# Kernel optimization log

Hardware: AMD Instinct MI355X
Metric: run time of the kernel (lower is better)

Reference implementation:

```python
import jax, jax.numpy as jnp
import numpy as np

N = 100000   # nodes
E = 400000   # edges (before self-loops)
G = 4000     # graphs in batch
F_IN = 32    # node_embedding
HID = 128    # hidden_channels
H = 3        # heads (hard-coded in module)
W3 = H * HID # 384, post-concat width
NC = 10      # num_classes
NL = 4       # num_layers
NEG_SLOPE = 0.2


def _lin(key, fan_in, fan_out):
    return jax.random.normal(key, (fan_in, fan_out), jnp.float32) * (1.0 / np.sqrt(fan_in))


def setup_inputs() -> dict:
    key = jax.random.key(0)
    ks = iter(jax.random.split(key, 40))
    x = jax.random.normal(next(ks), (N, F_IN), jnp.float32)
    edge_index = jax.random.randint(next(ks), (2, E), 0, N, dtype=jnp.int32)
    batch = jnp.sort(jax.random.randint(next(ks), (N,), 0, G, dtype=jnp.int32))
    inp = dict(x=x, edge_index=edge_index, batch=batch)
    # MLP stem
    inp['lin1_w'] = _lin(next(ks), F_IN, 2 * HID); inp['lin1_b'] = jnp.zeros((2 * HID,), jnp.float32)
    inp['lin2_w'] = _lin(next(ks), 2 * HID, HID);  inp['lin2_b'] = jnp.zeros((HID,), jnp.float32)
    # conv1: GATConv(HID -> HID, heads=3)
    inp['w0'] = _lin(next(ks), HID, W3)
    inp['as0'] = jax.random.normal(next(ks), (H, HID), jnp.float32) * 0.1
    inp['ad0'] = jax.random.normal(next(ks), (H, HID), jnp.float32) * 0.1
    inp['b0'] = jnp.zeros((W3,), jnp.float32)
    # remaining NL-1 convs: GATConv(W3 -> HID, heads=3), stacked
    inp['wl'] = jnp.stack([_lin(next(ks), W3, W3) for _ in range(NL - 1)])
    inp['asl'] = jax.random.normal(next(ks), (NL - 1, H, HID), jnp.float32) * 0.1
    inp['adl'] = jax.random.normal(next(ks), (NL - 1, H, HID), jnp.float32) * 0.1
    inp['bl'] = jnp.zeros((NL - 1, W3), jnp.float32)
    # batch norms (NL total, all width W3)
    inp['gamma'] = jnp.ones((NL, W3), jnp.float32)
    inp['beta'] = jnp.zeros((NL, W3), jnp.float32)
    # head
    inp['lin3_w'] = _lin(next(ks), W3, HID); inp['lin3_b'] = jnp.zeros((HID,), jnp.float32)
    inp['lin4_w'] = _lin(next(ks), HID, NC); inp['lin4_b'] = jnp.zeros((NC,), jnp.float32)
    return inp


def _gat(x, W, a_src, a_dst, bias, src, dst):
    # PyG GATConv, concat heads. x: [N, Fin]
    h = (x @ W).reshape(N, H, HID)                       # [N, H, C]
    es = jnp.einsum('nhc,hc->nh', h, a_src)              # [N, H]
    ed = jnp.einsum('nhc,hc->nh', h, a_dst)
    e = jax.nn.leaky_relu(es[src] + ed[dst], NEG_SLOPE)  # [Etot, H]
    m = jax.ops.segment_max(e, dst, num_segments=N)      # segment softmax over incoming edges
    p = jnp.exp(e - m[dst])
    s = jax.ops.segment_sum(p, dst, num_segments=N)
    alpha = p / s[dst]                                   # every node has a self-loop -> s>0
    out = jax.ops.segment_sum(alpha[:, :, None] * h[src], dst, num_segments=N)
    return out.reshape(N, W3) + bias


def _bn(x, g, b):
    mu = x.mean(0)
    var = x.var(0)
    return (x - mu) * jax.lax.rsqrt(var + 1e-5) * g + b


def reference(x, edge_index, batch, lin1_w, lin1_b, lin2_w, lin2_b,
              w0, as0, ad0, b0, wl, asl, adl, bl, gamma, beta,
              lin3_w, lin3_b, lin4_w, lin4_b):
    loop = jnp.arange(N, dtype=edge_index.dtype)
    src = jnp.concatenate([edge_index[0], loop])  # add_self_loops=True (PyG default)
    dst = jnp.concatenate([edge_index[1], loop])
    h = jax.nn.relu(x @ lin1_w + lin1_b)
    h = jax.nn.relu(h @ lin2_w + lin2_b)
    h = _gat(h, w0, as0, ad0, b0, src, dst)
    h = _bn(h, gamma[0], beta[0])
    for i in range(NL - 1):
        h = _gat(h, wl[i], asl[i], adl[i], bl[i], src, dst)
        h = _bn(h, gamma[i + 1], beta[i + 1])
    # global mean pool over graphs
    sums = jax.ops.segment_sum(h, batch, num_segments=G)
    cnt = jax.ops.segment_sum(jnp.ones((N,), h.dtype), batch, num_segments=G)
    g = sums / jnp.maximum(cnt, 1.0)[:, None]
    g = jax.nn.relu(g @ lin3_w + lin3_b)
    logits = g @ lin4_w + lin4_b
    return jax.nn.log_softmax(logits, axis=-1)
```

## Files before the change

kernel.cpp:

```cpp
#include <hip/hip_runtime.h>

#define NN      100000
#define NN2     100096
#define NE      400000
#define ETOT    500000
#define NG      4000
#define W3D     384
#define HIDD    128
#define NCLS    10
#define NSLICE  256

typedef unsigned short u16;
typedef unsigned int   u32;
typedef unsigned long long u64;
typedef __attribute__((ext_vector_type(8))) short short8;
typedef __attribute__((ext_vector_type(4))) float f32x4;

static __device__ __forceinline__ float bf2f(u16 u) {
  return __uint_as_float(((u32)u) << 16);
}
static __device__ __forceinline__ float bflo(u32 u) {
  return __uint_as_float(u << 16);
}
static __device__ __forceinline__ float bfhi(u32 u) {
  return __uint_as_float(u & 0xffff0000u);
}
static __device__ __forceinline__ u16 f2b(float f) {
  u32 u = __float_as_uint(f);
  u32 r = (u + 0x7fffu + ((u >> 16) & 1u)) >> 16;
  return (u16)r;
}

static __device__ __forceinline__ void llds16(const u16* g, u16* l) {
  __builtin_amdgcn_global_load_lds(
      (const __attribute__((address_space(1))) void*)(u64)(const void*)g,
      (__attribute__((address_space(3))) void*)(u64)(void*)l, 16, 0, 0);
}

__global__ void mg_zero_out(float* out, int n) {
  int i = blockIdx.x * 256 + threadIdx.x;
  if (i < n) out[i] = 0.f;
}

__global__ void mg_cvt_x(const float* __restrict__ x, u16* __restrict__ Xb) {
  int idx = blockIdx.x * 256 + threadIdx.x;
  if (idx >= NN2 * 64) return;
  int row = idx >> 6, col = idx & 63;
  Xb[idx] = (row < NN && col < 32) ? f2b(x[row * 32 + col]) : (u16)0;
}

__global__ void mg_transpose_pad(const float* __restrict__ in, u16* __restrict__ out,
                                 int K, int Nn, int Kpad) {
  int idx = blockIdx.x * 256 + threadIdx.x;
  if (idx >= Nn * Kpad) return;
  int n = idx / Kpad, k = idx - n * Kpad;
  out[idx] = (k < K) ? f2b(in[k * Nn + n]) : (u16)0;
}

__global__ void mg_fold_w(const u16* __restrict__ Wt, const float* __restrict__ scale,
                          const float* __restrict__ shift, u16* __restrict__ Wp,
                          float* __restrict__ bp) {
  __shared__ float red[128];
  int j = blockIdx.x, t = threadIdx.x;
  const u16* src = Wt + (size_t)j * W3D;
  u16* dst = Wp + (size_t)j * W3D;
  float acc = 0.f;
  for (int k = t; k < W3D; k += 128) {
    float w = bf2f(src[k]);
    dst[k] = f2b(w * scale[k]);
    acc += w * shift[k];
  }
  red[t] = acc; __syncthreads();
  for (int off = 64; off; off >>= 1) {
    if (t < off) red[t] += red[t + off];
    __syncthreads();
  }
  if (t == 0) bp[j] = red[0];
}

__global__ void mg_edge_histo(const int* __restrict__ ei, int* __restrict__ deg) {
  int e = blockIdx.x * 256 + threadIdx.x;
  if (e >= ETOT) return;
  int d = (e < NE) ? ei[NE + e] : (e - NE);
  atomicAdd(&deg[d], 1);
}

__global__ void mg_scan1(const int* __restrict__ in, int* __restrict__ bsum, int n) {
  __shared__ int sd[256];
  int tid = threadIdx.x;
  int base = blockIdx.x * 1024 + tid * 4;
  int s = 0;
#pragma unroll
  for (int j = 0; j < 4; ++j) { int i = base + j; if (i < n) s += in[i]; }
  sd[tid] = s; __syncthreads();
  for (int off = 128; off > 0; off >>= 1) {
    if (tid < off) sd[tid] += sd[tid + off];
    __syncthreads();
  }
  if (tid == 0) bsum[blockIdx.x] = sd[0];
}

__global__ void mg_scan2(int* __restrict__ bsum, int nb) {
  __shared__ int sd[256];
  int tid = threadIdx.x;
  int v = (tid < nb) ? bsum[tid] : 0;
  sd[tid] = v; __syncthreads();
  for (int off = 1; off < 256; off <<= 1) {
    int t = (tid >= off) ? sd[tid - off] : 0;
    __syncthreads();
    sd[tid] += t;
    __syncthreads();
  }
  if (tid < nb) bsum[tid] = sd[tid] - v;
}

__global__ void mg_scan3(const int* __restrict__ in, const int* __restrict__ bexcl,
                         int* __restrict__ out, int n) {
  __shared__ int sd[256];
  int tid = threadIdx.x;
  int base = blockIdx.x * 1024 + tid * 4;
  int loc[4]; int s = 0;
#pragma unroll
  for (int j = 0; j < 4; ++j) { int i = base + j; loc[j] = (i < n) ? in[i] : 0; s += loc[j]; }
  sd[tid] = s; __syncthreads();
  for (int off = 1; off < 256; off <<= 1) {
    int t = (tid >= off) ? sd[tid - off] : 0;
    __syncthreads();
    sd[tid] += t;
    __syncthreads();
  }
  int run = sd[tid] - s + bexcl[blockIdx.x];
#pragma unroll
  for (int j = 0; j < 4; ++j) {
    int i = base + j;
    if (i < n) { out[i] = run; run += loc[j]; if (i == n - 1) out[n] = run; }
  }
}

__global__ void mg_edge_scatter(const int* __restrict__ ei, int* __restrict__ fill,
                                int* __restrict__ colsrc) {
  int e = blockIdx.x * 256 + threadIdx.x;
  if (e >= ETOT) return;
  int s, d;
  if (e < NE) { s = ei[e]; d = ei[NE + e]; } else { s = e - NE; d = s; }
  int pos = atomicAdd(&fill[d], 1);
  colsrc[pos] = s;
}

__global__ void mg_graph_ptr(const int* __restrict__ batch, int* __restrict__ gptr) {
  int g = blockIdx.x * 256 + threadIdx.x;
  if (g > NG) return;
  if (g == NG) { gptr[NG] = NN; return; }
  int lo = 0, hi = NN;
  while (lo < hi) { int mid = (lo + hi) >> 1; if (batch[mid] < g) lo = mid + 1; else hi = mid; }
  gptr[g] = lo;
}

#define GBM 128
#define GBN 128
#define GBK 64
#define CP  136

__global__ __launch_bounds__(256) void mg_gemm(
    const u16* __restrict__ Ag, const u16* __restrict__ Bt,
    int Mstore, int Nn, int K,
    u16* __restrict__ Cb, const float* __restrict__ bias, int relu,
    const float* __restrict__ asrc, const float* __restrict__ adst,
    float* __restrict__ aes, float* __restrict__ aed) {
  __shared__ u16 lds[32768];
  int tid = threadIdx.x;
  int n0 = blockIdx.x * GBN, m0 = blockIdx.y * GBM;
  int lane = tid & 63, wv = tid >> 6;
  int mw = (wv & 1) * 64, nw = (wv >> 1) * 64;
  int lr = lane & 15, lq = lane >> 4;
  int sr = lane & 7, scl = lane >> 3;

  f32x4 acc[4][4];
#pragma unroll
  for (int mi = 0; mi < 4; ++mi)
#pragma unroll
    for (int ni = 0; ni < 4; ++ni) acc[mi][ni] = (f32x4){0.f, 0.f, 0.f, 0.f};

  const u16* aB = Ag + (size_t)m0 * K + scl * 8;
  const u16* bB = Bt + (size_t)n0 * K + scl * 8;
  int niter = K / GBK;

#pragma unroll
  for (int j = 0; j < 4; ++j) {
    int g = wv * 4 + j, grow = g * 8 + sr;
    llds16(aB + (size_t)grow * K, lds + g * 512);
    llds16(bB + (size_t)grow * K, lds + 16384 + g * 512);
  }

  for (int it = 0; it < niter; ++it) {
    __syncthreads();
    if (it + 1 < niter) {
      int k0 = (it + 1) * GBK, b = (it + 1) & 1;
#pragma unroll
      for (int j = 0; j < 4; ++j) {
        int g = wv * 4 + j, grow = g * 8 + sr;
        llds16(aB + (size_t)grow * K + k0, lds + b * 8192 + g * 512);
        llds16(bB + (size_t)grow * K + k0, lds + 16384 + b * 8192 + g * 512);
      }
    }
    const u16* Al = lds + (it & 1) * 8192;
    const u16* Bl = lds + 16384 + (it & 1) * 8192;
#pragma unroll
    for (int kk = 0; kk < GBK; kk += 32) {
      int ca = (kk >> 3) + lq;
      short8 af[4], bfr[4];
#pragma unroll
      for (int mi = 0; mi < 4; ++mi) {
        int r = mw + mi * 16 + lr;
        af[mi] = *(const short8*)(Al + (r >> 3) * 512 + ca * 64 + (r & 7) * 8);
      }
#pragma unroll
      for (int ni = 0; ni < 4; ++ni) {
        int r = nw + ni * 16 + lr;
        bfr[ni] = *(const short8*)(Bl + (r >> 3) * 512 + ca * 64 + (r & 7) * 8);
      }
#pragma unroll
      for (int mi = 0; mi < 4; ++mi)
#pragma unroll
        for (int ni = 0; ni < 4; ++ni)
          acc[mi][ni] = __builtin_amdgcn_mfma_f32_16x16x32_bf16(af[mi], bfr[ni], acc[mi][ni], 0, 0, 0);
    }
    __syncthreads();
  }

  float bvv[4];
#pragma unroll
  for (int ni = 0; ni < 4; ++ni)
    bvv[ni] = bias ? bias[n0 + nw + ni * 16 + lr] : 0.f;

#pragma unroll
  for (int mi = 0; mi < 4; ++mi)
#pragma unroll
    for (int ni = 0; ni < 4; ++ni) {
      int cl = nw + ni * 16 + lr;
      int rb = mw + mi * 16 + lq * 4;
#pragma unroll
      for (int r = 0; r < 4; ++r) {
        float v = acc[mi][ni][r] + bvv[ni];
        if (relu) v = fmaxf(v, 0.f);
        lds[(rb + r) * CP + cl] = f2b(v);
      }
    }
  __syncthreads();

  int rowl = tid >> 1, half = (tid & 1) * 64;
  const u16* src = lds + rowl * CP + half;
  uint4 creg[8];
#pragma unroll
  for (int j = 0; j < 8; ++j) creg[j] = *(const uint4*)(src + j * 8);
  u16* gout = Cb + (size_t)(m0 + rowl) * Nn + n0 + half;
#pragma unroll
  for (int j = 0; j < 8; ++j) *(uint4*)(gout + j * 8) = creg[j];

  if (aes) {
    const float* ap = asrc + n0 + half;
    const float* dp = adst + n0 + half;
    float se = 0.f, de = 0.f;
#pragma unroll
    for (int j = 0; j < 8; ++j) {
      float4 a0 = *(const float4*)(ap + j * 8);
      float4 a1 = *(const float4*)(ap + j * 8 + 4);
      float4 d0 = *(const float4*)(dp + j * 8);
      float4 d1 = *(const float4*)(dp + j * 8 + 4);
      uint4 rv = creg[j];
      float v0 = bflo(rv.x), v1 = bfhi(rv.x), v2 = bflo(rv.y), v3 = bfhi(rv.y);
      float v4 = bflo(rv.z), v5 = bfhi(rv.z), v6 = bflo(rv.w), v7 = bfhi(rv.w);
      se += v0 * a0.x + v1 * a0.y + v2 * a0.z + v3 * a0.w
          + v4 * a1.x + v5 * a1.y + v6 * a1.z + v7 * a1.w;
      de += v0 * d0.x + v1 * d0.y + v2 * d0.z + v3 * d0.w
          + v4 * d1.x + v5 * d1.y + v6 * d1.z + v7 * d1.w;
    }
    se += __shfl_xor(se, 1);
    de += __shfl_xor(de, 1);
    int row = m0 + rowl;
    if ((tid & 1) == 0 && row < Mstore) {
      aes[row * 4 + blockIdx.x] = se;
      aed[row * 4 + blockIdx.x] = de;
    }
  }
}

__global__ __launch_bounds__(256) void mg_aggregate(
    const u16* __restrict__ B, const float* __restrict__ es,
    const float* __restrict__ ed, const int* __restrict__ rowptr,
    const int* __restrict__ colsrc, const float* __restrict__ bias,
    u16* __restrict__ A, float* __restrict__ stats) {
  __shared__ float bS[4 * W3D];
  __shared__ float bQ[4 * W3D];
  int wv = threadIdx.x >> 6, lane = threadIdx.x & 63;
  if (lane < 48) {
    int h = lane >> 4;
    int cc = lane * 8;
    float4 bv0 = *(const float4*)(bias + cc);
    float4 bv1 = *(const float4*)(bias + cc + 4);
    float stS[8], stQ[8];
#pragma unroll
    for (int j = 0; j < 8; ++j) { stS[j] = 0.f; stQ[j] = 0.f; }
#pragma unroll
    for (int sub = 0; sub < 2; ++sub) {
      int n = blockIdx.x * 8 + wv * 2 + sub;
      int r0 = rowptr[n], r1 = rowptr[n + 1];
      float4 edv = *(const float4*)(ed + 4 * n);
      float4 esn = *(const float4*)(es + 4 * n);
      float s0 = esn.x + edv.x; s0 = (s0 > 0.f) ? s0 : 0.2f * s0;
      float s1 = esn.y + edv.y; s1 = (s1 > 0.f) ? s1 : 0.2f * s1;
      float s2 = esn.z + edv.z; s2 = (s2 > 0.f) ? s2 : 0.2f * s2;
      float mh  = (h == 0) ? s0 : ((h == 1) ? s1 : s2);
      float edh = (h == 0) ? edv.x : ((h == 1) ? edv.y : edv.z);
      float accv[8];
#pragma unroll
      for (int j = 0; j < 8; ++j) accv[j] = 0.f;
      float ssum = 0.f;
      int sA = __builtin_amdgcn_readfirstlane(colsrc[r0]);
      float4 evA = *(const float4*)(es + 4 * sA);
      uint4  rvA = *(const uint4*)(B + (size_t)sA * W3D + cc);
      float4 evB = evA; uint4 rvB = rvA;
      if (r0 + 1 < r1) {
        int sB = __builtin_amdgcn_readfirstlane(colsrc[r0 + 1]);
        evB = *(const float4*)(es + 4 * sB);
        rvB = *(const uint4*)(B + (size_t)sB * W3D + cc);
      }
      for (int r = r0; r < r1; ++r) {
        float4 ev = evA; uint4 rv = rvA;
        evA = evB; rvA = rvB;
        if (r + 2 < r1) {
          int sC = __builtin_amdgcn_readfirstlane(colsrc[r + 2]);
          evB = *(const float4*)(es + 4 * sC);
          rvB = *(const uint4*)(B + (size_t)sC * W3D + cc);
        }
        float e = ((h == 0) ? ev.x : ((h == 1) ? ev.y : ev.z)) + edh;
        e = (e > 0.f) ? e : 0.2f * e;
        float p = __expf(e - mh);
        ssum += p;
        accv[0] += p * bflo(rv.x); accv[1] += p * bfhi(rv.x);
        accv[2] += p * bflo(rv.y); accv[3] += p * bfhi(rv.y);
        accv[4] += p * bflo(rv.z); accv[5] += p * bfhi(rv.z);
        accv[6] += p * bflo(rv.w); accv[7] += p * bfhi(rv.w);
      }
      float inv = 1.0f / ssum;
      float v[8];
      v[0] = accv[0] * inv + bv0.x; v[1] = accv[1] * inv + bv0.y;
      v[2] = accv[2] * inv + bv0.z; v[3] = accv[3] * inv + bv0.w;
      v[4] = accv[4] * inv + bv1.x; v[5] = accv[5] * inv + bv1.y;
      v[6] = accv[6] * inv + bv1.z; v[7] = accv[7] * inv + bv1.w;
      uint4 st;
      st.x = (u32)f2b(v[0]) | ((u32)f2b(v[1]) << 16);
      st.y = (u32)f2b(v[2]) | ((u32)f2b(v[3]) << 16);
      st.z = (u32)f2b(v[4]) | ((u32)f2b(v[5]) << 16);
      st.w = (u32)f2b(v[6]) | ((u32)f2b(v[7]) << 16);
      *(uint4*)(A + (size_t)n * W3D + cc) = st;
#pragma unroll
      for (int j = 0; j < 8; ++j) { stS[j] += v[j]; stQ[j] += v[j] * v[j]; }
    }
    *(float4*)(bS + wv * W3D + cc)     = (float4){stS[0], stS[1], stS[2], stS[3]};
    *(float4*)(bS + wv * W3D + cc + 4) = (float4){stS[4], stS[5], stS[6], stS[7]};
    *(float4*)(bQ + wv * W3D + cc)     = (float4){stQ[0], stQ[1], stQ[2], stQ[3]};
    *(float4*)(bQ + wv * W3D + cc + 4) = (float4){stQ[4], stQ[5], stQ[6], stQ[7]};
  }
  __syncthreads();
  for (int t = threadIdx.x; t < W3D; t += 256) {
    float s = 0.f, q = 0.f;
#pragma unroll
    for (int w = 0; w < 4; ++w) { s += bS[w * W3D + t]; q += bQ[w * W3D + t]; }
    float* sl = stats + (size_t)(blockIdx.x & (NSLICE - 1)) * 768;
    atomicAdd(&sl[t], s);
    atomicAdd(&sl[W3D + t], q);
  }
}

__global__ void mg_bn_finalize(const float* __restrict__ stats, const float* __restrict__ gamma,
                               const float* __restrict__ beta, float* __restrict__ scale,
                               float* __restrict__ shift) {
  int c = threadIdx.x;
  float s = 0.f, q = 0.f;
  for (int b = 0; b < NSLICE; ++b) { s += stats[b * 768 + c]; q += stats[b * 768 + W3D + c]; }
  const float invN = 1.0f / (float)NN;
  float mu = s * invN;
  float var = fmaxf(q * invN - mu * mu, 0.f);
  float inv = rsqrtf(var + 1e-5f);
  float g = gamma[c], be = beta[c];
  scale[c] = g * inv;
  shift[c] = be - mu * g * inv;
}

__global__ void mg_pool(const u16* __restrict__ A, const float* __restrict__ scale,
                        const float* __restrict__ shift, const int* __restrict__ gptr,
                        float* __restrict__ pooled) {
  int g = blockIdx.x, c = threadIdx.x;
  int r0 = gptr[g], r1 = gptr[g + 1];
  float acc = 0.f;
  for (int n = r0; n < r1; ++n) acc += bf2f(A[(size_t)n * W3D + c]);
  int cnt = r1 - r0;
  float v = (cnt > 0) ? (acc / (float)cnt) * scale[c] + shift[c] : 0.f;
  pooled[g * W3D + c] = v;
}

__global__ void mg_head(const float* __restrict__ pooled, const float* __restrict__ w3,
                        const float* __restrict__ b3, const float* __restrict__ w4,
                        const float* __restrict__ b4, float* __restrict__ out) {
  __shared__ float p[W3D];
  __shared__ float g2[HIDD];
  __shared__ float lg[NCLS];
  int g = blockIdx.x, t = threadIdx.x;
  for (int i = t; i < W3D; i += 128) p[i] = pooled[g * W3D + i];
  __syncthreads();
  float acc = 0.f;
  for (int k = 0; k < W3D; ++k) acc += p[k] * w3[k * HIDD + t];
  g2[t] = fmaxf(acc + b3[t], 0.f);
  __syncthreads();
  if (t < NCLS) {
    float a = 0.f;
    for (int k = 0; k < HIDD; ++k) a += g2[k] * w4[k * NCLS + t];
    lg[t] = a + b4[t];
  }
  __syncthreads();
  if (t < NCLS) {
    float m = -1e30f;
#pragma unroll
    for (int j = 0; j < NCLS; ++j) m = fmaxf(m, lg[j]);
    float se = 0.f;
#pragma unroll
    for (int j = 0; j < NCLS; ++j) se += __expf(lg[j] - m);
    out[g * NCLS + t] = lg[t] - m - __logf(se);
  }
}

extern "C" void kernel_launch(void* const* d_in, const int* in_sizes, int n_in,
                              void* d_out, int out_size, void* d_ws, size_t ws_size,
                              hipStream_t stream) {
  const float* x     = (const float*)d_in[0];
  const int*   ei    = (const int*)d_in[1];
  const int*   batch = (const int*)d_in[2];
  const float* w1    = (const float*)d_in[3];
  const float* b1    = (const float*)d_in[4];
  const float* w2    = (const float*)d_in[5];
  const float* b2    = (const float*)d_in[6];
  const float* w0    = (const float*)d_in[7];
  const float* as0   = (const float*)d_in[8];
  const float* ad0   = (const float*)d_in[9];
  const float* b0    = (const float*)d_in[10];
  const float* wl    = (const float*)d_in[11];
  const float* asl   = (const float*)d_in[12];
  const float* adl   = (const float*)d_in[13];
  const float* bl    = (const float*)d_in[14];
  const float* gamma = (const float*)d_in[15];
  const float* beta  = (const float*)d_in[16];
  const float* w3    = (const float*)d_in[17];
  const float* b3    = (const float*)d_in[18];
  const float* w4    = (const float*)d_in[19];
  const float* b4    = (const float*)d_in[20];
  float* out = (float*)d_out;

  char* w = (char*)d_ws;
  auto alloc = [&](size_t bytes) -> void* {
    void* p = (void*)w;
    w += (bytes + 255) & ~(size_t)255;
    return p;
  };
  u16*   P      = (u16*)alloc((size_t)NN2 * W3D * 2);
  u16*   Q      = (u16*)alloc((size_t)NN2 * W3D * 2);
  float* es     = (float*)alloc((size_t)NN * 4 * 4);
  float* ed     = (float*)alloc((size_t)NN * 4 * 4);
  int*   deg    = (int*)alloc((size_t)NN * 4);
  int*   rowptr = (int*)alloc((size_t)(NN + 1) * 4);
  int*   fill   = (int*)alloc((size_t)NN * 4);
  int*   colsrc = (int*)alloc((size_t)ETOT * 4);
  int*   bsum   = (int*)alloc(256 * 4);
  float* stats  = (float*)alloc((size_t)NSLICE * 768 * 4);
  float* scale  = (float*)alloc(W3D * 4);
  float* shift  = (float*)alloc(W3D * 4);
  float* bprime = (float*)alloc(W3D * 4);
  int*   gptr   = (int*)alloc((size_t)(NG + 1) * 4);
  float* pooled = (float*)alloc((size_t)NG * W3D * 4);
  u16*   W1T    = (u16*)alloc(256 * 64 * 2);
  u16*   W2T    = (u16*)alloc(128 * 256 * 2);
  u16*   W0T    = (u16*)alloc(384 * 128 * 2);
  u16*   WlT    = (u16*)alloc((size_t)3 * 384 * 384 * 2);
  u16*   WpT    = (u16*)alloc((size_t)384 * 384 * 2);
  u16*   Xb     = Q;

  if ((size_t)(w - (char*)d_ws) > ws_size) {
    mg_zero_out<<<(out_size + 255) / 256, 256, 0, stream>>>(out, out_size);
    return;
  }

  mg_cvt_x<<<(NN2 * 64 + 255) / 256, 256, 0, stream>>>(x, Xb);
  mg_transpose_pad<<<(256 * 64 + 255) / 256, 256, 0, stream>>>(w1, W1T, 32, 256, 64);
  mg_transpose_pad<<<(128 * 256 + 255) / 256, 256, 0, stream>>>(w2, W2T, 256, 128, 256);
  mg_transpose_pad<<<(384 * 128 + 255) / 256, 256, 0, stream>>>(w0, W0T, 128, 384, 128);
  for (int i = 0; i < 3; ++i)
    mg_transpose_pad<<<(384 * 384 + 255) / 256, 256, 0, stream>>>(
        wl + (size_t)i * 384 * 384, WlT + (size_t)i * 384 * 384, 384, 384, 384);

  hipMemsetAsync(deg, 0, (size_t)NN * 4, stream);
  mg_edge_histo<<<(ETOT + 255) / 256, 256, 0, stream>>>(ei, deg);
  int nb = (NN + 1023) / 1024;
  mg_scan1<<<nb, 256, 0, stream>>>(deg, bsum, NN);
  mg_scan2<<<1, 256, 0, stream>>>(bsum, nb);
  mg_scan3<<<nb, 256, 0, stream>>>(deg, bsum, rowptr, NN);
  hipMemcpyAsync(fill, rowptr, (size_t)NN * 4, hipMemcpyDeviceToDevice, stream);
  mg_edge_scatter<<<(ETOT + 255) / 256, 256, 0, stream>>>(ei, fill, colsrc);
  mg_graph_ptr<<<(NG + 1 + 255) / 256, 256, 0, stream>>>(batch, gptr);

  dim3 blk(256);
  int mtiles = NN2 / GBM;

  mg_gemm<<<dim3(2, mtiles), blk, 0, stream>>>(Xb, W1T, NN, 256, 64,
                                               P, b1, 1,
                                               nullptr, nullptr, nullptr, nullptr);
  mg_gemm<<<dim3(1, mtiles), blk, 0, stream>>>(P, W2T, NN, 128, 256,
                                               Q, b2, 1,
                                               nullptr, nullptr, nullptr, nullptr);

  for (int i = 0; i < 4; ++i) {
    int K = (i == 0) ? 128 : 384;
    const u16* Bt;
    const float* bi_g = nullptr;
    if (i == 0) {
      Bt = W0T;
    } else {
      mg_fold_w<<<384, 128, 0, stream>>>(WlT + (size_t)(i - 1) * 384 * 384,
                                         scale, shift, WpT, bprime);
      Bt = WpT;
      bi_g = bprime;
    }
    const float* as = (i == 0) ? as0 : (asl + (size_t)(i - 1) * 384);
    const float* ad = (i == 0) ? ad0 : (adl + (size_t)(i - 1) * 384);
    const float* bi = (i == 0) ? b0  : (bl  + (size_t)(i - 1) * 384);
    hipMemsetAsync(stats, 0, (size_t)NSLICE * 768 * 4, stream);
    mg_gemm<<<dim3(3, mtiles), blk, 0, stream>>>(Q, Bt, NN, W3D, K,
                                                 P, bi_g, 0,
                                                 as, ad, es, ed);
    mg_aggregate<<<NN / 8, blk, 0, stream>>>(P, es, ed, rowptr, colsrc, bi, Q, stats);
    mg_bn_finalize<<<1, 384, 0, stream>>>(stats, gamma + (size_t)i * W3D,
                                          beta + (size_t)i * W3D, scale, shift);
  }

  mg_pool<<<NG, 384, 0, stream>>>(Q, scale, shift, gptr, pooled);
  mg_head<<<NG, 128, 0, stream>>>(pooled, w3, b3, w4, b4, out);
}
```

Before: 1.117 ms.

## Halve GEMM K-tile, relayout LDS staging, and drop the trailing per-iteration barrier

The bf16 MFMA GEMM K-tile shrinks from 64 to 32 and LDS use drops to about 34KB, which may allow more resident blocks per CU. Global-to-LDS staging now places 16 rows per segment with a different address layout, so fragment reads become contiguous per lane. The output staging pitch changes to 130, and the second __syncthreads inside the K loop is removed. That leaves only one barrier per iteration, so the prefetch into the other buffer can race with reads of the previous buffer if ordering is not guaranteed.

New measurement: 1.118 ms. No clear change (+0.1%).

```diff
diff --git a/kernel.cpp b/kernel.cpp
--- a/kernel.cpp
+++ b/kernel.cpp
@@ -158,8 +158,8 @@
 
 #define GBM 128
 #define GBN 128
-#define GBK 64
-#define CP  136
+#define GBK 32
+#define CP  130
 
 __global__ __launch_bounds__(256) void mg_gemm(
     const u16* __restrict__ Ag, const u16* __restrict__ Bt,
@@ -167,13 +167,13 @@
     u16* __restrict__ Cb, const float* __restrict__ bias, int relu,
     const float* __restrict__ asrc, const float* __restrict__ adst,
     float* __restrict__ aes, float* __restrict__ aed) {
-  __shared__ u16 lds[32768];
+  __shared__ u16 lds[17408];
   int tid = threadIdx.x;
   int n0 = blockIdx.x * GBN, m0 = blockIdx.y * GBM;
   int lane = tid & 63, wv = tid >> 6;
   int mw = (wv & 1) * 64, nw = (wv >> 1) * 64;
   int lr = lane & 15, lq = lane >> 4;
-  int sr = lane & 7, scl = lane >> 3;
+  int rr = lane & 15, cc4 = lane >> 4;
 
   f32x4 acc[4][4];
 #pragma unroll
@@ -181,15 +181,15 @@
 #pragma unroll
     for (int ni = 0; ni < 4; ++ni) acc[mi][ni] = (f32x4){0.f, 0.f, 0.f, 0.f};
 
-  const u16* aB = Ag + (size_t)m0 * K + scl * 8;
-  const u16* bB = Bt + (size_t)n0 * K + scl * 8;
-  int niter = K / GBK;
-
-#pragma unroll
-  for (int j = 0; j < 4; ++j) {
-    int g = wv * 4 + j, grow = g * 8 + sr;
-    llds16(aB + (size_t)grow * K, lds + g * 512);
-    llds16(bB + (size_t)grow * K, lds + 16384 + g * 512);
+  const u16* aB = Ag + (size_t)m0 * K + cc4 * 8;
+  const u16* bB = Bt + (size_t)n0 * K + cc4 * 8;
+  int niter = K >> 5;
+
+#pragma unroll
+  for (int j = 0; j < 2; ++j) {
+    int sg = wv * 2 + j, grow = sg * 16 + rr;
+    llds16(aB + (size_t)grow * K, lds + sg * 512);
+    llds16(bB + (size_t)grow * K, lds + 8192 + sg * 512);
   }
 
   for (int it = 0; it < niter; ++it) {
@@ -197,36 +197,28 @@
     if (it + 1 < niter) {
       int k0 = (it + 1) * GBK, b = (it + 1) & 1;
 #pragma unroll
-      for (int j = 0; j < 4; ++j) {
-        int g = wv * 4 + j, grow = g * 8 + sr;
-        llds16(aB + (size_t)grow * K + k0, lds + b * 8192 + g * 512);
-        llds16(bB + (size_t)grow * K + k0, lds + 16384 + b * 8192 + g * 512);
+      for (int j = 0; j < 2; ++j) {
+        int sg = wv * 2 + j, grow = sg * 16 + rr;
+        llds16(aB + (size_t)grow * K + k0, lds + b * 4096 + sg * 512);
+        llds16(bB + (size_t)grow * K + k0, lds + 8192 + b * 4096 + sg * 512);
       }
     }
-    const u16* Al = lds + (it & 1) * 8192;
-    const u16* Bl = lds + 16384 + (it & 1) * 8192;
-#pragma unroll
-    for (int kk = 0; kk < GBK; kk += 32) {
-      int ca = (kk >> 3) + lq;
-      short8 af[4], bfr[4];
-#pragma unroll
-      for (int mi = 0; mi < 4; ++mi) {
-        int r = mw + mi * 16 + lr;
-        af[mi] = *(const short8*)(Al + (r >> 3) * 512 + ca * 64 + (r & 7) * 8);
-      }
-#pragma unroll
-      for (int ni = 0; ni < 4; ++ni) {
-        int r = nw + ni * 16 + lr;
-        bfr[ni] = *(const short8*)(Bl + (r >> 3) * 512 + ca * 64 + (r & 7) * 8);
-      }
-#pragma unroll
-      for (int mi = 0; mi < 4; ++mi)
-#pragma unroll
-        for (int ni = 0; ni < 4; ++ni)
-          acc[mi][ni] = __builtin_amdgcn_mfma_f32_16x16x32_bf16(af[mi], bfr[ni], acc[mi][ni], 0, 0, 0);
-    }
-    __syncthreads();
-  }
+    const u16* Al = lds + (it & 1) * 4096;
+    const u16* Bl = lds + 8192 + (it & 1) * 4096;
+    short8 af[4], bfr[4];
+#pragma unroll
+    for (int mi = 0; mi < 4; ++mi)
+      af[mi] = *(const short8*)(Al + ((mw >> 4) + mi) * 512 + lq * 128 + lr * 8);
+#pragma unroll
+    for (int ni = 0; ni < 4; ++ni)
+      bfr[ni] = *(const short8*)(Bl + ((nw >> 4) + ni) * 512 + lq * 128 + lr * 8);
+#pragma unroll
+    for (int mi = 0; mi < 4; ++mi)
+#pragma unroll
+      for (int ni = 0; ni < 4; ++ni)
+        acc[mi][ni] = __builtin_amdgcn_mfma_f32_16x16x32_bf16(af[mi], bfr[ni], acc[mi][ni], 0, 0, 0);
+  }
+  __syncthreads();
 
   float bvv[4];
 #pragma unroll
```

## Replace double-buffered LDS direct loads with register-staged single-buffer GEMM pipeline

Applied to the files above, without the earlier changes.

The GEMM no longer uses global_load_lds into a double-buffered 64KB LDS tile. It prefetches the next K tile into registers, stores it into a single-buffered LDS region after a barrier, and bumps launch bounds to allow three blocks per CU. The smaller LDS footprint is meant to raise occupancy and hide memory latency across blocks, at the cost of an extra barrier per iteration and more register pressure. The aggregate launch now passes a literal block size, which looks cosmetic.

Measured after the change: 1.529 ms. +36.9%, slower.

```diff
diff --git a/kernel.cpp b/kernel.cpp
--- a/kernel.cpp
+++ b/kernel.cpp
@@ -29,12 +29,6 @@
   u32 u = __float_as_uint(f);
   u32 r = (u + 0x7fffu + ((u >> 16) & 1u)) >> 16;
   return (u16)r;
-}
-
-static __device__ __forceinline__ void llds16(const u16* g, u16* l) {
-  __builtin_amdgcn_global_load_lds(
-      (const __attribute__((address_space(1))) void*)(u64)(const void*)g,
-      (__attribute__((address_space(3))) void*)(u64)(void*)l, 16, 0, 0);
 }
 
 __global__ void mg_zero_out(float* out, int n) {
@@ -161,13 +155,13 @@
 #define GBK 64
 #define CP  136
 
-__global__ __launch_bounds__(256) void mg_gemm(
+__global__ __launch_bounds__(256, 3) void mg_gemm(
     const u16* __restrict__ Ag, const u16* __restrict__ Bt,
     int Mstore, int Nn, int K,
     u16* __restrict__ Cb, const float* __restrict__ bias, int relu,
     const float* __restrict__ asrc, const float* __restrict__ adst,
     float* __restrict__ aes, float* __restrict__ aed) {
-  __shared__ u16 lds[32768];
+  __shared__ u16 lds[17408];
   int tid = threadIdx.x;
   int n0 = blockIdx.x * GBN, m0 = blockIdx.y * GBM;
   int lane = tid & 63, wv = tid >> 6;
@@ -183,28 +177,34 @@
 
   const u16* aB = Ag + (size_t)m0 * K + scl * 8;
   const u16* bB = Bt + (size_t)n0 * K + scl * 8;
-  int niter = K / GBK;
-
+  int niter = K >> 6;
+
+  uint4 ra[4], rb[4];
 #pragma unroll
   for (int j = 0; j < 4; ++j) {
-    int g = wv * 4 + j, grow = g * 8 + sr;
-    llds16(aB + (size_t)grow * K, lds + g * 512);
-    llds16(bB + (size_t)grow * K, lds + 16384 + g * 512);
+    int grow = (wv * 4 + j) * 8 + sr;
+    ra[j] = *(const uint4*)(aB + (size_t)grow * K);
+    rb[j] = *(const uint4*)(bB + (size_t)grow * K);
   }
 
   for (int it = 0; it < niter; ++it) {
     __syncthreads();
+#pragma unroll
+    for (int j = 0; j < 4; ++j) {
+      int g = wv * 4 + j;
+      *(uint4*)(lds + g * 512 + lane * 8) = ra[j];
+      *(uint4*)(lds + 8192 + g * 512 + lane * 8) = rb[j];
+    }
     if (it + 1 < niter) {
-      int k0 = (it + 1) * GBK, b = (it + 1) & 1;
+      int k0 = (it + 1) * GBK;
 #pragma unroll
       for (int j = 0; j < 4; ++j) {
-        int g = wv * 4 + j, grow = g * 8 + sr;
-        llds16(aB + (size_t)grow * K + k0, lds + b * 8192 + g * 512);
-        llds16(bB + (size_t)grow * K + k0, lds + 16384 + b * 8192 + g * 512);
+        int grow = (wv * 4 + j) * 8 + sr;
+        ra[j] = *(const uint4*)(aB + (size_t)grow * K + k0);
+        rb[j] = *(const uint4*)(bB + (size_t)grow * K + k0);
       }
     }
-    const u16* Al = lds + (it & 1) * 8192;
-    const u16* Bl = lds + 16384 + (it & 1) * 8192;
+    __syncthreads();
 #pragma unroll
     for (int kk = 0; kk < GBK; kk += 32) {
       int ca = (kk >> 3) + lq;
@@ -212,12 +212,12 @@
 #pragma unroll
       for (int mi = 0; mi < 4; ++mi) {
         int r = mw + mi * 16 + lr;
-        af[mi] = *(const short8*)(Al + (r >> 3) * 512 + ca * 64 + (r & 7) * 8);
+        af[mi] = *(const short8*)(lds + (r >> 3) * 512 + ca * 64 + (r & 7) * 8);
       }
 #pragma unroll
       for (int ni = 0; ni < 4; ++ni) {
         int r = nw + ni * 16 + lr;
-        bfr[ni] = *(const short8*)(Bl + (r >> 3) * 512 + ca * 64 + (r & 7) * 8);
+        bfr[ni] = *(const short8*)(lds + 8192 + (r >> 3) * 512 + ca * 64 + (r & 7) * 8);
       }
 #pragma unroll
       for (int mi = 0; mi < 4; ++mi)
@@ -225,8 +225,8 @@
         for (int ni = 0; ni < 4; ++ni)
           acc[mi][ni] = __builtin_amdgcn_mfma_f32_16x16x32_bf16(af[mi], bfr[ni], acc[mi][ni], 0, 0, 0);
     }
-    __syncthreads();
-  }
+  }
+  __syncthreads();
 
   float bvv[4];
 #pragma unroll
@@ -238,12 +238,12 @@
 #pragma unroll
     for (int ni = 0; ni < 4; ++ni) {
       int cl = nw + ni * 16 + lr;
-      int rb = mw + mi * 16 + lq * 4;
+      int rb2 = mw + mi * 16 + lq * 4;
 #pragma unroll
       for (int r = 0; r < 4; ++r) {
         float v = acc[mi][ni][r] + bvv[ni];
         if (relu) v = fmaxf(v, 0.f);
-        lds[(rb + r) * CP + cl] = f2b(v);
+        lds[(rb2 + r) * CP + cl] = f2b(v);
       }
     }
   __syncthreads();
@@ -536,7 +536,7 @@
     mg_gemm<<<dim3(3, mtiles), blk, 0, stream>>>(Q, Bt, NN, W3D, K,
                                                  P, bi_g, 0,
                                                  as, ad, es, ed);
-    mg_aggregate<<<NN / 8, blk, 0, stream>>>(P, es, ed, rowptr, colsrc, bi, Q, stats);
+    mg_aggregate<<<NN / 8, 256, 0, stream>>>(P, es, ed, rowptr, colsrc, bi, Q, stats);
     mg_bn_finalize<<<1, 384, 0, stream>>>(stats, gamma + (size_t)i * W3D,
                                           beta + (size_t)i * W3D, scale, shift);
   }
```
